# Optimization experiments

Measured on AMD Instinct MI355X. Metric: run time of the kernel, lower is better.

Reference implementation:

```python
import jax, jax.numpy as jnp
import numpy as np

D = 2048
H = 16
HD = D // H
FF = 4 * D
EPS = 1e-5


def layernorm(x, scale, shift):
    mean = jnp.mean(x, axis=-1, keepdims=True)
    var = jnp.mean((x - mean) ** 2, axis=-1, keepdims=True)  # unbiased=False
    return scale * (x - mean) / jnp.sqrt(var + EPS) + shift


def setup_inputs() -> dict:
    key = jax.random.key(0)
    ks = jax.random.split(key, 12)
    s = 0.02
    return {
        "x": jax.random.normal(ks[0], (2, 2048, D), dtype=jnp.float32),
        "ln1_scale": jnp.ones((D,), jnp.float32),
        "ln1_shift": jnp.zeros((D,), jnp.float32),
        "wq": jax.random.normal(ks[1], (D, D), jnp.float32) * s,
        "bq": jnp.zeros((D,), jnp.float32),
        "wk": jax.random.normal(ks[2], (D, D), jnp.float32) * s,
        "bk": jnp.zeros((D,), jnp.float32),
        "wv": jax.random.normal(ks[3], (D, D), jnp.float32) * s,
        "bv": jnp.zeros((D,), jnp.float32),
        "wo": jax.random.normal(ks[4], (D, D), jnp.float32) * s,
        "bo": jnp.zeros((D,), jnp.float32),
        "ln2_scale": jnp.ones((D,), jnp.float32),
        "ln2_shift": jnp.zeros((D,), jnp.float32),
        "w1": jax.random.normal(ks[5], (D, FF), jnp.float32) * s,
        "b1": jnp.zeros((FF,), jnp.float32),
        "w2": jax.random.normal(ks[6], (FF, D), jnp.float32) * s,
        "b2": jnp.zeros((D,), jnp.float32),
    }


def block(x, ln1_scale, ln1_shift, wq, bq, wk, bk, wv, bv, wo, bo,
          ln2_scale, ln2_shift, w1, b1, w2, b2):
    B, S, _ = x.shape
    h = layernorm(x, ln1_scale, ln1_shift)
    q = (h @ wq + bq).reshape(B, S, H, HD).transpose(0, 2, 1, 3)  # [B,H,S,hd]
    k = (h @ wk + bk).reshape(B, S, H, HD).transpose(0, 2, 1, 3)
    v = (h @ wv + bv).reshape(B, S, H, HD).transpose(0, 2, 1, 3)
    scores = jnp.einsum("bhqd,bhkd->bhqk", q, k) / jnp.sqrt(jnp.float32(HD))
    causal = jnp.tril(jnp.ones((S, S), dtype=bool))
    scores = jnp.where(causal[None, None], scores, -jnp.inf)
    attn = jax.nn.softmax(scores, axis=-1)
    ctx = jnp.einsum("bhqk,bhkd->bhqd", attn, v)
    ctx = ctx.transpose(0, 2, 1, 3).reshape(B, S, D)
    x = x + (ctx @ wo + bo)
    h2 = layernorm(x, ln2_scale, ln2_shift)
    ffn = jax.nn.gelu(h2 @ w1 + b1, approximate=False) @ w2 + b2
    return x + ffn


def reference(x, ln1_scale, ln1_shift, wq, bq, wk, bk, wv, bv, wo, bo,
              ln2_scale, ln2_shift, w1, b1, w2, b2):
    return block(x, ln1_scale, ln1_shift, wq, bq, wk, bk, wv, bv, wo, bo,
                 ln2_scale, ln2_shift, w1, b1, w2, b2)
```

## Files before the change

### kernel.cpp

```cpp
#include <hip/hip_runtime.h>
#include <hip/hip_bf16.h>
#include <math.h>

namespace {

constexpr int Dm  = 2048;
constexpr int FFm = 8192;
constexpr int SEQ = 2048;
constexpr int HDm = 128;
constexpr int MR  = 4096;
constexpr int QW  = 3 * Dm;

typedef __bf16 bf16_t;
typedef __bf16 bf16x8 __attribute__((ext_vector_type(8)));
typedef float  f32x4  __attribute__((ext_vector_type(4)));

typedef __attribute__((address_space(1))) const void as1_void;
typedef __attribute__((address_space(3))) void as3_void;

__device__ __forceinline__ void gload_lds16(const void* g, void* l) {
  __builtin_amdgcn_global_load_lds((as1_void*)g, (as3_void*)l, 16, 0, 0);
}

__global__ __launch_bounds__(256)
void ln_kernel(const float* __restrict__ x, const float* __restrict__ sc,
               const float* __restrict__ sh, bf16_t* __restrict__ out)
{
  const int row = blockIdx.x;
  const int tid = threadIdx.x;
  const float4* xr = (const float4*)(x + (size_t)row * Dm);
  float4 v0 = xr[tid*2], v1 = xr[tid*2+1];
  float s  = v0.x+v0.y+v0.z+v0.w + v1.x+v1.y+v1.z+v1.w;
  float s2 = v0.x*v0.x+v0.y*v0.y+v0.z*v0.z+v0.w*v0.w
           + v1.x*v1.x+v1.y*v1.y+v1.z*v1.z+v1.w*v1.w;
  #pragma unroll
  for (int off = 32; off; off >>= 1) { s += __shfl_xor(s, off); s2 += __shfl_xor(s2, off); }
  __shared__ float red[8];
  if ((tid & 63) == 0) { red[(tid>>6)*2] = s; red[(tid>>6)*2+1] = s2; }
  __syncthreads();
  s  = red[0]+red[2]+red[4]+red[6];
  s2 = red[1]+red[3]+red[5]+red[7];
  const float mean = s * (1.f/Dm);
  const float var  = fmaxf(s2 * (1.f/Dm) - mean*mean, 0.f);
  const float rstd = rsqrtf(var + 1e-5f);
  const float4* scp = (const float4*)sc;
  const float4* shp = (const float4*)sh;
  float4 sc0 = scp[tid*2], sc1 = scp[tid*2+1];
  float4 sh0 = shp[tid*2], sh1 = shp[tid*2+1];
  __attribute__((aligned(16))) bf16_t ob[8];
  ob[0] = (bf16_t)((v0.x-mean)*rstd*sc0.x + sh0.x);
  ob[1] = (bf16_t)((v0.y-mean)*rstd*sc0.y + sh0.y);
  ob[2] = (bf16_t)((v0.z-mean)*rstd*sc0.z + sh0.z);
  ob[3] = (bf16_t)((v0.w-mean)*rstd*sc0.w + sh0.w);
  ob[4] = (bf16_t)((v1.x-mean)*rstd*sc1.x + sh1.x);
  ob[5] = (bf16_t)((v1.y-mean)*rstd*sc1.y + sh1.y);
  ob[6] = (bf16_t)((v1.z-mean)*rstd*sc1.z + sh1.z);
  ob[7] = (bf16_t)((v1.w-mean)*rstd*sc1.w + sh1.w);
  *(uint4*)(out + (size_t)row*Dm + tid*8) = *(const uint4*)ob;
}

__global__ __launch_bounds__(256)
void wconv4(const float* __restrict__ wq, const float* __restrict__ wk,
            const float* __restrict__ wv, const float* __restrict__ wo,
            bf16_t* __restrict__ dst)
{
  const int z = blockIdx.z;
  const float* W = (z == 0) ? wq : (z == 1) ? wk : (z == 2) ? wv : wo;
  bf16_t* WT = dst + (size_t)z * Dm * Dm;
  __shared__ float tile[32][33];
  const int tx = threadIdx.x & 31, ty = threadIdx.x >> 5;
  const int nb = blockIdx.x * 32, kb = blockIdx.y * 32;
  #pragma unroll
  for (int p = 0; p < 4; ++p)
    tile[ty+8*p][tx] = W[(size_t)(kb+ty+8*p)*Dm + nb + tx];
  __syncthreads();
  #pragma unroll
  for (int p = 0; p < 4; ++p)
    WT[(size_t)(nb+ty+8*p)*Dm + kb + tx] = (bf16_t)tile[tx][ty+8*p];
}

__global__ __launch_bounds__(256)
void wconv_t(const float* __restrict__ W, bf16_t* __restrict__ WT, int K, int N)
{
  __shared__ float tile[32][33];
  const int tx = threadIdx.x & 31, ty = threadIdx.x >> 5;
  const int nb = blockIdx.x * 32, kb = blockIdx.y * 32;
  #pragma unroll
  for (int p = 0; p < 4; ++p)
    tile[ty+8*p][tx] = W[(size_t)(kb+ty+8*p)*N + nb + tx];
  __syncthreads();
  #pragma unroll
  for (int p = 0; p < 4; ++p)
    WT[(size_t)(nb+ty+8*p)*K + kb + tx] = (bf16_t)tile[tx][ty+8*p];
}

__global__ void bias_concat(const float* __restrict__ bq, const float* __restrict__ bk,
                            const float* __restrict__ bv, float* __restrict__ o)
{
  int i = blockIdx.x*256 + threadIdx.x;
  o[i] = bq[i]; o[Dm+i] = bk[i]; o[2*Dm+i] = bv[i];
}

__global__ __launch_bounds__(256)
void vtrans(const bf16_t* __restrict__ qkv, bf16_t* __restrict__ vT)
{
  __shared__ bf16_t tile[32][33];
  const int tx = threadIdx.x & 31, ty = threadIdx.x >> 5;
  const int s0 = blockIdx.x*32, d0 = blockIdx.y*32, bh = blockIdx.z;
  const int b = bh >> 4, h = bh & 15;
  const bf16_t* src = qkv + (size_t)(b*SEQ)*QW + 2*Dm + h*HDm;
  #pragma unroll
  for (int p = 0; p < 4; ++p)
    tile[ty+8*p][tx] = src[(size_t)(s0+ty+8*p)*QW + d0 + tx];
  __syncthreads();
  bf16_t* dst = vT + (size_t)bh*HDm*SEQ;
  #pragma unroll
  for (int p = 0; p < 4; ++p)
    dst[(size_t)(d0+ty+8*p)*SEQ + s0 + tx] = tile[tx][ty+8*p];
}

template<int MODE>
__global__ __launch_bounds__(512, 2)
void gemm8p(const bf16_t* __restrict__ A, const bf16_t* __restrict__ BT,
            const float* __restrict__ bias,
            void* __restrict__ Cout, void* __restrict__ Cout2,
            int Ndim, int Kslice, int Kstride, int gn)
{
  const int gm = (int)gridDim.x / gn;
  const int cm = gm >> 1, cn = gn >> 2;
  const int c = blockIdx.x & 7;
  const int idx = blockIdx.x >> 3;
  const int mi = idx / cn, ni = idx - mi*cn;
  const int m0 = ((c >> 2)*cm + mi) * 256;
  const int n0 = ((c & 3)*cn + ni) * 256;
  const int kOff = blockIdx.y * Kslice;
  const int tid = threadIdx.x;
  const int lane = tid & 63;
  const int w = tid >> 6;
  const int wr = w >> 2, wc = w & 3;
  const int lr = lane & 15, kg = lane >> 4;

  __shared__ __attribute__((aligned(16))) bf16_t lds[65536];

  f32x4 acc[8][4] = {};

  const int r1   = tid >> 3;
  const int blk1 = (tid & 7) ^ (r1 & 7);
  const size_t rowoff = (size_t)64 * Kstride;
  const bf16_t* pA0 = A  + (size_t)(m0 + r1)*Kstride       + kOff + blk1*8;
  const bf16_t* pA1 = A  + (size_t)(m0 + 128 + r1)*Kstride + kOff + blk1*8;
  const bf16_t* pB0 = BT + (size_t)(n0 + r1)*Kstride       + kOff + blk1*8;
  const bf16_t* pB1 = BT + (size_t)(n0 + 128 + r1)*Kstride + kOff + blk1*8;
  bf16_t* const d0 = lds + (size_t)tid*8;

#define STG(p, region) do { \
    gload_lds16((p), d0 + (size_t)(region)*8192); \
    gload_lds16((p) + rowoff, d0 + (size_t)(region)*8192 + 4096); \
    (p) += 64; } while (0)

  auto readA = [&](int buf, int mh, bf16x8* f) {
    const bf16_t* base = lds + (buf*4 + wr)*8192;
    #pragma unroll
    for (int ml = 0; ml < 4; ++ml)
      #pragma unroll
      for (int kk = 0; kk < 2; ++kk) {
        const int row = mh*64 + ml*16 + lr;
        f[ml*2+kk] = *(const bf16x8*)(base + row*64 + (((kk*4+kg) ^ (row&7))*8));
      }
  };
  auto readB = [&](int buf, int nh, bf16x8* f) {
    const bf16_t* base = lds + (buf*4 + 2 + (wc>>1))*8192;
    #pragma unroll
    for (int nl = 0; nl < 2; ++nl)
      #pragma unroll
      for (int kk = 0; kk < 2; ++kk) {
        const int row = (wc&1)*64 + nh*32 + nl*16 + lr;
        f[nl*2+kk] = *(const bf16x8*)(base + row*64 + (((kk*4+kg) ^ (row&7))*8));
      }
  };
  auto mfma16 = [&](int mh, int nh, const bf16x8* Af, const bf16x8* Bf) {
    #pragma unroll
    for (int ml = 0; ml < 4; ++ml)
      #pragma unroll
      for (int nl = 0; nl < 2; ++nl)
        #pragma unroll
        for (int kk = 0; kk < 2; ++kk)
          acc[mh*4+ml][nh*2+nl] =
            __builtin_amdgcn_mfma_f32_16x16x32_bf16(Af[ml*2+kk], Bf[nl*2+kk],
                                                    acc[mh*4+ml][nh*2+nl], 0, 0, 0);
  };

  bf16x8 Af0[8], Af1[8], Bf0[4], Bf1[4];

  STG(pA0, 0); STG(pA1, 1); STG(pB0, 2); STG(pB1, 3);
  STG(pA0, 4); STG(pA1, 5);
  asm volatile("s_waitcnt vmcnt(4)" ::: "memory");
  __builtin_amdgcn_s_barrier();
  readA(0, 0, Af0);

  const int NT = Kslice >> 6;
  for (int t = 0; t < NT; ++t) {
    const int buf = t & 1, nbuf = buf ^ 1;
    const bool s1 = (t + 1 < NT), s2 = (t + 2 < NT);

    readB(buf, 0, Bf0);
    readB(buf, 1, Bf1);
    readA(buf, 1, Af1);
    if (s1) { STG(pB0, nbuf*4 + 2); STG(pB1, nbuf*4 + 3); }
    __builtin_amdgcn_s_barrier();
    __builtin_amdgcn_s_setprio(1);
    mfma16(0, 0, Af0, Bf0);
    mfma16(0, 1, Af0, Bf1);
    __builtin_amdgcn_s_setprio(0);
    asm volatile("s_waitcnt lgkmcnt(0)");
    __builtin_amdgcn_s_barrier();

    if (s2) { STG(pA0, buf*4 + 0); STG(pA1, buf*4 + 1); }
    __builtin_amdgcn_s_barrier();
    if (s2)      asm volatile("s_waitcnt vmcnt(8)" ::: "memory");
    else if (s1) asm volatile("s_waitcnt vmcnt(4)" ::: "memory");
    if (s1) readA(nbuf, 0, Af0);
    __builtin_amdgcn_s_setprio(1);
    mfma16(1, 0, Af1, Bf0);
    mfma16(1, 1, Af1, Bf1);
    __builtin_amdgcn_s_setprio(0);
    if (s2)      asm volatile("s_waitcnt vmcnt(4)" ::: "memory");
    else         asm volatile("s_waitcnt vmcnt(0)" ::: "memory");
    __builtin_amdgcn_s_barrier();
  }
#undef STG

  const int cr0 = m0 + wr*128 + kg*4;
  if constexpr (MODE == 0 || MODE == 1) {
    __syncthreads();
    #pragma unroll
    for (int nf = 0; nf < 4; ++nf) {
      const int col = wc*64 + nf*16 + lr;
      const float bv = bias[n0 + col];
      #pragma unroll
      for (int mf = 0; mf < 8; ++mf) {
        #pragma unroll
        for (int jj = 0; jj < 4; ++jj) {
          float v = acc[mf][nf][jj] + bv;
          if constexpr (MODE == 1) v = 0.5f*v*(1.f + erff(v*0.70710678118f));
          const int row = wr*128 + mf*16 + kg*4 + jj;
          const int adr = row*256 + (((col >> 3) ^ (row & 7)) << 3) + (col & 7);
          lds[adr] = (bf16_t)v;
        }
      }
    }
    __syncthreads();
    bf16_t* outp = (bf16_t*)Cout;
    #pragma unroll
    for (int i = 0; i < 16; ++i) {
      const int s = tid + i*512;
      const int row = s >> 5, ch = s & 31;
      uint4 vv = *(const uint4*)(lds + row*256 + ((ch ^ (row & 7)) << 3));
      *(uint4*)(outp + (size_t)(m0 + row)*Ndim + n0 + ch*8) = vv;
    }
  } else {
    float* pout = (float*)(blockIdx.y ? Cout2 : Cout);
    #pragma unroll
    for (int nf = 0; nf < 4; ++nf) {
      const int col = n0 + wc*64 + nf*16 + lr;
      #pragma unroll
      for (int mf = 0; mf < 8; ++mf) {
        const int rbase = cr0 + mf*16;
        #pragma unroll
        for (int jj = 0; jj < 4; ++jj)
          pout[(size_t)(rbase + jj)*Ndim + col] = acc[mf][nf][jj];
      }
    }
  }
}

__global__ __launch_bounds__(256)
void splitk_reduce(const float* __restrict__ p0, const float* __restrict__ p1,
                   const float* __restrict__ bias, const float* __restrict__ resid,
                   float* __restrict__ out, int Ndim)
{
  const size_t e = ((size_t)blockIdx.x*256 + threadIdx.x) * 4;
  float4 a = *(const float4*)(p0 + e);
  float4 b = *(const float4*)(p1 + e);
  float4 r = *(const float4*)(resid + e);
  float4 bv = *(const float4*)(bias + (int)(e & (size_t)(Ndim - 1)));
  float4 o;
  o.x = a.x + b.x + bv.x + r.x;
  o.y = a.y + b.y + bv.y + r.y;
  o.z = a.z + b.z + bv.z + r.z;
  o.w = a.w + b.w + bv.w + r.w;
  *(float4*)(out + e) = o;
}

__global__ __launch_bounds__(512, 2)
void flash_attn3(const bf16_t* __restrict__ qkv, const bf16_t* __restrict__ vT,
                 bf16_t* __restrict__ ctx)
{
  const int bid = blockIdx.x;
  const int bh  = (bid & 7) + 8 * ((bid >> 3) & 3);
  const int qi  = 7 - (bid >> 5);
  const int b = bh >> 4, h = bh & 15;
  const int Q0 = qi * 256;
  const int tid = threadIdx.x;
  const int lane = tid & 63;
  const int w = tid >> 6;
  const int lr = lane & 15, kg = lane >> 4;
  const int q0w = Q0 + w * 32;

  __shared__ __attribute__((aligned(16))) bf16_t Ks[64*128];
  __shared__ __attribute__((aligned(16))) bf16_t Vs[128*64];
  __shared__ __attribute__((aligned(16))) bf16_t Plds[8*2048];

  const bf16_t* kbase = qkv + (size_t)(b*SEQ)*QW + Dm + h*HDm;
  const bf16_t* vbase = vT + (size_t)bh*HDm*SEQ;

  bf16x8 qf[2][4];
  #pragma unroll
  for (int rt = 0; rt < 2; ++rt) {
    const bf16_t* qb = qkv + (size_t)(b*SEQ + q0w + rt*16 + lr)*QW + h*HDm;
    #pragma unroll
    for (int g = 0; g < 4; ++g)
      qf[rt][g] = *(const bf16x8*)(qb + g*32 + kg*8);
  }

  const float scl = 0.08838834764831845f * 1.44269504089f;
  float mrow[2][4], lsum[2][4];
  f32x4 oacc[2][8];
  #pragma unroll
  for (int rt = 0; rt < 2; ++rt) {
    #pragma unroll
    for (int j = 0; j < 4; ++j) { mrow[rt][j] = -INFINITY; lsum[rt][j] = 0.f; }
    #pragma unroll
    for (int dt = 0; dt < 8; ++dt) oacc[rt][dt] = (f32x4){0.f,0.f,0.f,0.f};
  }

  auto stage = [&](int k0) {
    #pragma unroll
    for (int i = 0; i < 2; ++i) {
      const int s = tid + i*512;
      const int row = s >> 4, sl = s & 15;
      gload_lds16(kbase + (size_t)(k0 + row)*QW + (sl ^ (row & 7))*8, Ks + s*8);
    }
    #pragma unroll
    for (int i = 0; i < 2; ++i) {
      const int s = tid + i*512;
      const int row = s >> 3, sl = s & 7;
      gload_lds16(vbase + (size_t)row*SEQ + k0 + (sl ^ (row & 7))*8, Vs + s*8);
    }
  };

  const int nsteps = (Q0 + 256) >> 6;
  stage(0);
  for (int t = 0; t < nsteps; ++t) {
    const int k0 = t * 64;
    __syncthreads();
    if (k0 < q0w + 32) {
      f32x4 sa[2][4];
      #pragma unroll
      for (int rt = 0; rt < 2; ++rt)
        #pragma unroll
        for (int ct = 0; ct < 4; ++ct) sa[rt][ct] = (f32x4){0.f,0.f,0.f,0.f};
      #pragma unroll
      for (int ct = 0; ct < 4; ++ct) {
        const int krow = ct*16 + lr;
        #pragma unroll
        for (int g = 0; g < 4; ++g) {
          bf16x8 kf = *(const bf16x8*)(Ks + krow*128 + ((4*g + kg) ^ (krow & 7))*8);
          sa[0][ct] = __builtin_amdgcn_mfma_f32_16x16x32_bf16(qf[0][g], kf, sa[0][ct], 0, 0, 0);
          sa[1][ct] = __builtin_amdgcn_mfma_f32_16x16x32_bf16(qf[1][g], kf, sa[1][ct], 0, 0, 0);
        }
      }
      #pragma unroll
      for (int rt = 0; rt < 2; ++rt)
        #pragma unroll
        for (int ct = 0; ct < 4; ++ct)
          #pragma unroll
          for (int j = 0; j < 4; ++j) sa[rt][ct][j] *= scl;
      if (k0 + 63 > q0w) {
        #pragma unroll
        for (int ct = 0; ct < 4; ++ct) {
          const int kidx = k0 + ct*16 + lr;
          #pragma unroll
          for (int rt = 0; rt < 2; ++rt)
            #pragma unroll
            for (int j = 0; j < 4; ++j) {
              const int qidx = q0w + rt*16 + kg*4 + j;
              if (kidx > qidx) sa[rt][ct][j] = -INFINITY;
            }
        }
      }
      #pragma unroll
      for (int rt = 0; rt < 2; ++rt) {
        #pragma unroll
        for (int j = 0; j < 4; ++j) {
          const int prow = kg*4 + j;
          float x0 = sa[rt][0][j], x1 = sa[rt][1][j], x2 = sa[rt][2][j], x3 = sa[rt][3][j];
          float v = fmaxf(fmaxf(x0, x1), fmaxf(x2, x3));
          v = fmaxf(v, __shfl_xor(v, 1));
          v = fmaxf(v, __shfl_xor(v, 2));
          v = fmaxf(v, __shfl_xor(v, 4));
          v = fmaxf(v, __shfl_xor(v, 8));
          const float mn = fmaxf(mrow[rt][j], v);
          const float alpha = exp2f(mrow[rt][j] - mn);
          mrow[rt][j] = mn;
          float p0 = exp2f(x0 - mn), p1 = exp2f(x1 - mn);
          float p2 = exp2f(x2 - mn), p3 = exp2f(x3 - mn);
          float ss = (p0 + p1) + (p2 + p3);
          ss += __shfl_xor(ss, 1);
          ss += __shfl_xor(ss, 2);
          ss += __shfl_xor(ss, 4);
          ss += __shfl_xor(ss, 8);
          lsum[rt][j] = lsum[rt][j]*alpha + ss;
          #pragma unroll
          for (int dt = 0; dt < 8; ++dt) oacc[rt][dt][j] *= alpha;
          const int base = w*2048 + rt*1024 + prow*64;
          const int sw = (prow & 7) << 3;
          Plds[(base + ( 0 + lr)) ^ sw] = (bf16_t)p0;
          Plds[(base + (16 + lr)) ^ sw] = (bf16_t)p1;
          Plds[(base + (32 + lr)) ^ sw] = (bf16_t)p2;
          Plds[(base + (48 + lr)) ^ sw] = (bf16_t)p3;
        }
      }
      bf16x8 pf[2][2];
      {
        const int sw = (lr & 7) << 3;
        #pragma unroll
        for (int rt = 0; rt < 2; ++rt) {
          pf[rt][0] = *(const bf16x8*)(Plds + ((w*2048 + rt*1024 + lr*64 +      kg*8) ^ sw));
          pf[rt][1] = *(const bf16x8*)(Plds + ((w*2048 + rt*1024 + lr*64 + 32 + kg*8) ^ sw));
        }
      }
      #pragma unroll
      for (int dt = 0; dt < 8; ++dt) {
        const int vrow = dt*16 + lr;
        #pragma unroll
        for (int kc = 0; kc < 2; ++kc) {
          bf16x8 vf = *(const bf16x8*)(Vs + vrow*64 + ((4*kc + kg) ^ (vrow & 7))*8);
          oacc[0][dt] = __builtin_amdgcn_mfma_f32_16x16x32_bf16(pf[0][kc], vf, oacc[0][dt], 0, 0, 0);
          oacc[1][dt] = __builtin_amdgcn_mfma_f32_16x16x32_bf16(pf[1][kc], vf, oacc[1][dt], 0, 0, 0);
        }
      }
    }
    __syncthreads();
    if (t + 1 < nsteps) stage((t + 1) * 64);
  }

  #pragma unroll
  for (int rt = 0; rt < 2; ++rt) {
    bf16_t* cb = ctx + (size_t)(b*SEQ + q0w + rt*16 + kg*4)*Dm + h*HDm;
    #pragma unroll
    for (int j = 0; j < 4; ++j) {
      const float inv = 1.f / lsum[rt][j];
      #pragma unroll
      for (int dt = 0; dt < 8; ++dt)
        cb[(size_t)j*Dm + dt*16 + lr] = (bf16_t)(oacc[rt][dt][j] * inv);
    }
  }
}

}

extern "C" void kernel_launch(void* const* d_in, const int* in_sizes, int n_in,
                              void* d_out, int out_size, void* d_ws, size_t ws_size,
                              hipStream_t stream)
{
  const float* x   = (const float*)d_in[0];
  const float* g1  = (const float*)d_in[1];
  const float* s1  = (const float*)d_in[2];
  const float* wq  = (const float*)d_in[3];
  const float* bq  = (const float*)d_in[4];
  const float* wk  = (const float*)d_in[5];
  const float* bk  = (const float*)d_in[6];
  const float* wv  = (const float*)d_in[7];
  const float* bv  = (const float*)d_in[8];
  const float* wo  = (const float*)d_in[9];
  const float* bo  = (const float*)d_in[10];
  const float* g2  = (const float*)d_in[11];
  const float* s2  = (const float*)d_in[12];
  const float* w1  = (const float*)d_in[13];
  const float* b1  = (const float*)d_in[14];
  const float* w2  = (const float*)d_in[15];
  const float* b2  = (const float*)d_in[16];
  float* out = (float*)d_out;

  char* p = (char*)d_ws;
  bf16_t* wqkvT = (bf16_t*)p;  p += (size_t)QW*Dm*2;
  bf16_t* woT   = (bf16_t*)p;  p += (size_t)Dm*Dm*2;
  bf16_t* w1T   = (bf16_t*)p;  p += (size_t)FFm*Dm*2;
  bf16_t* w2T   = (bf16_t*)p;  p += (size_t)Dm*FFm*2;
  float*  bqkv  = (float*)p;   p += (size_t)QW*4;
  bf16_t* hbuf  = (bf16_t*)p;  p += (size_t)MR*Dm*2;
  bf16_t* qkv   = (bf16_t*)p;  p += (size_t)MR*QW*2;
  bf16_t* vTb   = (bf16_t*)p;  p += (size_t)32*HDm*SEQ*2;
  bf16_t* ctx   = (bf16_t*)p;  p += (size_t)MR*Dm*2;
  float*  x1    = (float*)p;   p += (size_t)MR*Dm*4;
  bf16_t* ffn1  = qkv;
  float*  prj0  = (float*)qkv;
  float*  prj1  = (float*)qkv + (size_t)MR*Dm;
  float*  f2p0  = (float*)w1T;
  float*  f2p1  = (float*)wqkvT;

  wconv4<<<dim3(Dm/32, Dm/32, 4), 256, 0, stream>>>(wq, wk, wv, wo, wqkvT);
  wconv_t<<<dim3(FFm/32, Dm/32), 256, 0, stream>>>(w1, w1T, Dm, FFm);
  wconv_t<<<dim3(Dm/32, FFm/32), 256, 0, stream>>>(w2, w2T, FFm, Dm);
  bias_concat<<<dim3(Dm/256), 256, 0, stream>>>(bq, bk, bv, bqkv);

  ln_kernel<<<dim3(MR), 256, 0, stream>>>(x, g1, s1, hbuf);
  gemm8p<0><<<dim3((QW/256)*(MR/256), 1), 512, 0, stream>>>(
      hbuf, wqkvT, bqkv, qkv, nullptr, QW, Dm, Dm, QW/256);
  vtrans<<<dim3(SEQ/32, HDm/32, 32), 256, 0, stream>>>(qkv, vTb);
  flash_attn3<<<dim3(256), 512, 0, stream>>>(qkv, vTb, ctx);
  gemm8p<3><<<dim3((Dm/256)*(MR/256), 2), 512, 0, stream>>>(
      ctx, woT, nullptr, prj0, prj1, Dm, Dm/2, Dm, Dm/256);
  splitk_reduce<<<dim3(MR*Dm/1024), 256, 0, stream>>>(prj0, prj1, bo, x, x1, Dm);
  ln_kernel<<<dim3(MR), 256, 0, stream>>>(x1, g2, s2, hbuf);
  gemm8p<1><<<dim3((FFm/256)*(MR/256), 1), 512, 0, stream>>>(
      hbuf, w1T, b1, ffn1, nullptr, FFm, Dm, Dm, FFm/256);
  gemm8p<3><<<dim3((Dm/256)*(MR/256), 2), 512, 0, stream>>>(
      ffn1, w2T, nullptr, f2p0, f2p1, Dm, FFm/2, FFm, Dm/256);
  splitk_reduce<<<dim3(MR*Dm/1024), 256, 0, stream>>>(f2p0, f2p1, b2, x1, out, Dm);
}
```

Before: 725.0 us.

## Restructure GEMM main loop into 8-phase ping-pong schedule with remapped warp tiles

The 256x256 GEMM tile loop changes from a 64-K-step, two-phase schedule to a 128-K-step loop with eight phases. Each phase pairs a small LDS fragment read and a global-to-LDS stage with one 16-MFMA quadrant, separated by barriers. The warp-to-subtile mapping also changes so each warp covers interleaved 64x32 pieces of every 128x128 quadrant instead of one contiguous 128x64 region, and the epilogue indexing is updated to match. The goal is to spread LDS reads and global loads more evenly across MFMA work and reduce stalls. In exchange it adds many barriers, keeps duplicate fragment registers (more VGPR pressure), and requires Kslice to be a multiple of 128.

After: 720.2 us. About the same (-0.7%).

```diff
diff --git a/kernel.cpp b/kernel.cpp
--- a/kernel.cpp
+++ b/kernel.cpp
@@ -159,26 +159,27 @@
     (p) += 64; } while (0)
 
   auto readA = [&](int buf, int mh, bf16x8* f) {
-    const bf16_t* base = lds + (buf*4 + wr)*8192;
+    const bf16_t* base = lds + (buf*4 + mh)*8192;
     #pragma unroll
     for (int ml = 0; ml < 4; ++ml)
       #pragma unroll
       for (int kk = 0; kk < 2; ++kk) {
-        const int row = mh*64 + ml*16 + lr;
+        const int row = wr*64 + ml*16 + lr;
         f[ml*2+kk] = *(const bf16x8*)(base + row*64 + (((kk*4+kg) ^ (row&7))*8));
       }
   };
   auto readB = [&](int buf, int nh, bf16x8* f) {
-    const bf16_t* base = lds + (buf*4 + 2 + (wc>>1))*8192;
+    const bf16_t* base = lds + (buf*4 + 2 + nh)*8192;
     #pragma unroll
     for (int nl = 0; nl < 2; ++nl)
       #pragma unroll
       for (int kk = 0; kk < 2; ++kk) {
-        const int row = (wc&1)*64 + nh*32 + nl*16 + lr;
+        const int row = wc*32 + nl*16 + lr;
         f[nl*2+kk] = *(const bf16x8*)(base + row*64 + (((kk*4+kg) ^ (row&7))*8));
       }
   };
   auto mfma16 = [&](int mh, int nh, const bf16x8* Af, const bf16x8* Bf) {
+    __builtin_amdgcn_s_setprio(1);
     #pragma unroll
     for (int ml = 0; ml < 4; ++ml)
       #pragma unroll
@@ -188,62 +189,74 @@
           acc[mh*4+ml][nh*2+nl] =
             __builtin_amdgcn_mfma_f32_16x16x32_bf16(Af[ml*2+kk], Bf[nl*2+kk],
                                                     acc[mh*4+ml][nh*2+nl], 0, 0, 0);
+    __builtin_amdgcn_s_setprio(0);
   };
 
+#define BAR() __builtin_amdgcn_s_barrier()
+
   bf16x8 Af0[8], Af1[8], Bf0[4], Bf1[4];
+  bf16x8 Af0b[8], Af1b[8], Bf0b[4], Bf1b[4];
 
   STG(pA0, 0); STG(pA1, 1); STG(pB0, 2); STG(pB1, 3);
-  STG(pA0, 4); STG(pA1, 5);
-  asm volatile("s_waitcnt vmcnt(4)" ::: "memory");
-  __builtin_amdgcn_s_barrier();
-  readA(0, 0, Af0);
-
-  const int NT = Kslice >> 6;
-  for (int t = 0; t < NT; ++t) {
-    const int buf = t & 1, nbuf = buf ^ 1;
-    const bool s1 = (t + 1 < NT), s2 = (t + 2 < NT);
-
-    readB(buf, 0, Bf0);
-    readB(buf, 1, Bf1);
-    readA(buf, 1, Af1);
-    if (s1) { STG(pB0, nbuf*4 + 2); STG(pB1, nbuf*4 + 3); }
-    __builtin_amdgcn_s_barrier();
-    __builtin_amdgcn_s_setprio(1);
-    mfma16(0, 0, Af0, Bf0);
-    mfma16(0, 1, Af0, Bf1);
-    __builtin_amdgcn_s_setprio(0);
-    asm volatile("s_waitcnt lgkmcnt(0)");
-    __builtin_amdgcn_s_barrier();
-
-    if (s2) { STG(pA0, buf*4 + 0); STG(pA1, buf*4 + 1); }
-    __builtin_amdgcn_s_barrier();
-    if (s2)      asm volatile("s_waitcnt vmcnt(8)" ::: "memory");
-    else if (s1) asm volatile("s_waitcnt vmcnt(4)" ::: "memory");
-    if (s1) readA(nbuf, 0, Af0);
-    __builtin_amdgcn_s_setprio(1);
-    mfma16(1, 0, Af1, Bf0);
-    mfma16(1, 1, Af1, Bf1);
-    __builtin_amdgcn_s_setprio(0);
-    if (s2)      asm volatile("s_waitcnt vmcnt(4)" ::: "memory");
-    else         asm volatile("s_waitcnt vmcnt(0)" ::: "memory");
-    __builtin_amdgcn_s_barrier();
+  STG(pA0, 4); STG(pA1, 5); STG(pB0, 6); STG(pB1, 7);
+  asm volatile("s_waitcnt vmcnt(8)" ::: "memory");
+  BAR();
+
+  const int NITER = Kslice >> 7;
+  for (int j = 0; j < NITER; ++j) {
+    const bool s2 = (j + 1 < NITER);
+
+    readA(0, 0, Af0); readB(0, 0, Bf0);
+    BAR(); mfma16(0, 0, Af0, Bf0); BAR();
+
+    readB(0, 1, Bf1);
+    if (s2) STG(pA0, 0);
+    BAR(); mfma16(0, 1, Af0, Bf1); BAR();
+
+    readA(0, 1, Af1);
+    if (s2) STG(pB0, 2);
+    BAR(); mfma16(1, 1, Af1, Bf1);
+    if (s2) asm volatile("s_waitcnt vmcnt(4)" ::: "memory");
+    else    asm volatile("s_waitcnt vmcnt(0)" ::: "memory");
+    BAR();
+
+    readA(1, 0, Af0b);
+    if (s2) { STG(pA1, 1); STG(pB1, 3); }
+    BAR(); mfma16(1, 0, Af1, Bf0); BAR();
+
+    readB(1, 0, Bf0b);
+    BAR(); mfma16(0, 0, Af0b, Bf0b); BAR();
+
+    readB(1, 1, Bf1b);
+    if (s2) { STG(pA0, 4); STG(pB0, 6); }
+    BAR(); mfma16(0, 1, Af0b, Bf1b); BAR();
+
+    readA(1, 1, Af1b);
+    if (s2) STG(pB1, 7);
+    BAR(); mfma16(1, 1, Af1b, Bf1b); BAR();
+
+    if (s2) STG(pA1, 5);
+    BAR(); mfma16(1, 0, Af1b, Bf0b);
+    if (s2) asm volatile("s_waitcnt vmcnt(8)" ::: "memory");
+    else    asm volatile("s_waitcnt vmcnt(0)" ::: "memory");
+    BAR();
   }
 #undef STG
-
-  const int cr0 = m0 + wr*128 + kg*4;
+#undef BAR
+
   if constexpr (MODE == 0 || MODE == 1) {
     __syncthreads();
     #pragma unroll
-    for (int nf = 0; nf < 4; ++nf) {
-      const int col = wc*64 + nf*16 + lr;
+    for (int NF = 0; NF < 4; ++NF) {
+      const int col = (NF>>1)*128 + wc*32 + (NF&1)*16 + lr;
       const float bv = bias[n0 + col];
       #pragma unroll
-      for (int mf = 0; mf < 8; ++mf) {
+      for (int MF = 0; MF < 8; ++MF) {
         #pragma unroll
         for (int jj = 0; jj < 4; ++jj) {
-          float v = acc[mf][nf][jj] + bv;
+          float v = acc[MF][NF][jj] + bv;
           if constexpr (MODE == 1) v = 0.5f*v*(1.f + erff(v*0.70710678118f));
-          const int row = wr*128 + mf*16 + kg*4 + jj;
+          const int row = (MF>>2)*128 + wr*64 + (MF&3)*16 + kg*4 + jj;
           const int adr = row*256 + (((col >> 3) ^ (row & 7)) << 3) + (col & 7);
           lds[adr] = (bf16_t)v;
         }
@@ -261,14 +274,14 @@
   } else {
     float* pout = (float*)(blockIdx.y ? Cout2 : Cout);
     #pragma unroll
-    for (int nf = 0; nf < 4; ++nf) {
-      const int col = n0 + wc*64 + nf*16 + lr;
-      #pragma unroll
-      for (int mf = 0; mf < 8; ++mf) {
-        const int rbase = cr0 + mf*16;
+    for (int NF = 0; NF < 4; ++NF) {
+      const int col = n0 + (NF>>1)*128 + wc*32 + (NF&1)*16 + lr;
+      #pragma unroll
+      for (int MF = 0; MF < 8; ++MF) {
+        const int rbase = m0 + (MF>>2)*128 + wr*64 + (MF&3)*16 + kg*4;
         #pragma unroll
         for (int jj = 0; jj < 4; ++jj)
-          pout[(size_t)(rbase + jj)*Ndim + col] = acc[mf][nf][jj];
+          pout[(size_t)(rbase + jj)*Ndim + col] = acc[MF][NF][jj];
       }
     }
   }
```
